# Kernel optimization log

Measured on AMD Instinct MI355X. Metric: run time of the kernel, lower is better.

Reference implementation:

```python
import jax, jax.numpy as jnp
import numpy as np

MODEL_DIM = 2048
HEAD_DIM = 64
STATE_DIM = 128
EXPAND = 2
CHUNK = 64
INNER = EXPAND * MODEL_DIM          # 4096
NHEADS = INNER // HEAD_DIM          # 64
IN_PROJ = INNER + 2 * STATE_DIM + NHEADS  # 4416
B_SZ = 2
SEQ = 4096


def segsum(x):
    """Stable segment sum: x (..., T) -> (..., T, T) with -inf above diagonal."""
    T = x.shape[-1]
    mask_strict = jnp.tril(jnp.ones((T, T), dtype=bool), -1)
    # element [d, e] = x[d] on strictly-lower triangle, 0 elsewhere
    xt = jnp.where(mask_strict, x[..., :, None], 0.0)
    seg = jnp.cumsum(xt, axis=-2)
    mask = jnp.tril(jnp.ones((T, T), dtype=bool), 0)
    return jnp.where(mask, seg, -jnp.inf)


def ssd(x, A, B, C, chunk):
    """Mamba-2 SSD. x:(b,L,h,p), A:(b,L,h), B/C:(b,L,n) shared over heads."""
    b, L, h, p = x.shape
    n = B.shape[-1]
    c = L // chunk
    x = x.reshape(b, c, chunk, h, p)
    A = A.reshape(b, c, chunk, h).transpose(0, 3, 1, 2)  # (b,h,c,l)
    B = B.reshape(b, c, chunk, n)
    C = C.reshape(b, c, chunk, n)

    A_cs = jnp.cumsum(A, axis=-1)                        # (b,h,c,l)
    Lm = jnp.exp(segsum(A))                              # (b,h,c,l,l)
    # 1. diagonal (intra-chunk) output
    Y_diag = jnp.einsum('bcln,bcsn,bhcls,bcshp->bclhp', C, B, Lm, x)
    # 2. per-chunk states
    decay_states = jnp.exp(A_cs[..., -1:] - A_cs)        # (b,h,c,l)
    states = jnp.einsum('bcln,bhcl,bclhp->bchpn', B, decay_states, x)
    states = jnp.concatenate([jnp.zeros_like(states[:, :1]), states], axis=1)
    # 3. inter-chunk recurrence
    A_chunk = jnp.pad(A_cs[..., -1], ((0, 0), (0, 0), (1, 0)))   # (b,h,c+1)
    decay_chunk = jnp.exp(segsum(A_chunk))               # (b,h,c+1,c+1)
    new_states = jnp.einsum('bhzc,bchpn->bzhpn', decay_chunk, states)
    states_prev, final_state = new_states[:, :-1], new_states[:, -1]
    # 4. state -> output
    Y_off = jnp.einsum('bcln,bchpn,bhcl->bclhp', C, states_prev, jnp.exp(A_cs))
    Y = (Y_diag + Y_off).reshape(b, L, h, p)
    return Y, final_state


def setup_inputs() -> dict:
    key = jax.random.key(0)
    ks = jax.random.split(key, 6)
    u = jax.random.normal(ks[0], (B_SZ, SEQ, MODEL_DIM), jnp.float32)
    W_in = jax.random.normal(ks[1], (IN_PROJ, MODEL_DIM), jnp.float32) * 0.02
    b_in = jnp.zeros((IN_PROJ,), jnp.float32)
    W_out = jax.random.normal(ks[2], (MODEL_DIM, INNER), jnp.float32) * 0.02
    b_out = jnp.zeros((MODEL_DIM,), jnp.float32)
    # A_log = log(uniform(1, 16)) per Mamba-2 init
    A_log = jnp.log(jax.random.uniform(ks[3], (NHEADS,), jnp.float32, 1.0, 16.0))
    # dt_bias = inv-softplus of dt ~ loguniform(1e-3, 1e-1)
    dt = jnp.exp(jax.random.uniform(ks[4], (NHEADS,), jnp.float32)
                 * (np.log(0.1) - np.log(0.001)) + np.log(0.001))
    dt = jnp.clip(dt, 1e-4, None)
    dt_bias = dt + jnp.log(-jnp.expm1(-dt))
    return {'u': u, 'W_in': W_in, 'b_in': b_in, 'W_out': W_out,
            'b_out': b_out, 'A_log': A_log, 'dt_bias': dt_bias}


def reference(u, W_in, b_in, W_out, b_out, A_log, dt_bias):
    xBCdt = u @ W_in.T + b_in                       # (b, L, IN_PROJ)
    x, Bm, Cm, dt = jnp.split(
        xBCdt, [INNER, INNER + STATE_DIM, INNER + 2 * STATE_DIM], axis=-1)
    A = -jnp.exp(A_log)                             # (h,)
    dt = jax.nn.softplus(dt + dt_bias)              # (b, L, h)
    x = x.reshape(B_SZ, SEQ, NHEADS, HEAD_DIM)
    y, final_state = ssd(x * dt[..., None], A * dt, Bm, Cm, CHUNK)
    y = y.reshape(B_SZ, SEQ, INNER)
    y = y @ W_out.T + b_out
    return y, final_state
```

## Files before the change

kernel.cpp:

```cpp
#include <hip/hip_runtime.h>
#include <hip/hip_bf16.h>

typedef __hip_bfloat16 bf16;
typedef __attribute__((ext_vector_type(8))) short short8;
typedef __attribute__((ext_vector_type(4))) float f32x4;

#define MODEL_DIM 2048
#define INNER     4096
#define NHEADS    64
#define HEAD_DIM  64
#define STATE_DIM 128
#define IN_PROJ   4416
#define NPAD      4608
#define BSZ       2
#define SEQ       4096
#define CHUNKL    64
#define NTOK      (BSZ*SEQ)
#define NCHUNK    (SEQ/CHUNKL)

#define WAITV0() asm volatile("s_waitcnt vmcnt(0)" ::: "memory")
#define BAR()    __builtin_amdgcn_s_barrier()
#define SCHEDB() __builtin_amdgcn_sched_barrier(0)
#define WAITLG(N) do { asm volatile("s_waitcnt lgkmcnt(" #N ")" ::: "memory"); SCHEDB(); } while (0)

#define SWZ(x) ((x) ^ ((((x) >> 7) & 7) << 4))

static __device__ __forceinline__ void gload_lds16(const bf16* g, bf16* l) {
  __builtin_amdgcn_global_load_lds((const __attribute__((address_space(1))) void*)g,
                                   (__attribute__((address_space(3))) void*)l, 16, 0, 0);
}

static __device__ __forceinline__ unsigned lds_u32(const void* p) {
  return (unsigned)(unsigned long long)(const __attribute__((address_space(3))) char*)p;
}

static __device__ __forceinline__ short8 ds_read128(unsigned addr) {
  short8 r;
  asm volatile("ds_read_b128 %0, %1" : "=v"(r) : "v"(addr));
  return r;
}

static __device__ __forceinline__ void stage_unit(const bf16* __restrict__ P, int K,
                                                  int blockRow, int kt,
                                                  char* region, int unit, int t) {
  int o = unit * 8192 + (t << 4);
  int lb = SWZ(o);
  int row = lb >> 7, colb = lb & 127;
  gload_lds16(P + (size_t)(blockRow + row) * K + kt + (colb >> 1), (bf16*)(region + o));
}

#define MFMA_BLK(MLO, MHI, NLO, NHI)                                                    \
  __builtin_amdgcn_s_setprio(1);                                                       \
  _Pragma("unroll") for (int mf = (MLO); mf < (MHI); ++mf)                             \
    _Pragma("unroll") for (int nf = (NLO); nf < (NHI); ++nf)                           \
      _Pragma("unroll") for (int ks = 0; ks < 2; ++ks)                                 \
        acc[mf][nf] = __builtin_amdgcn_mfma_f32_16x16x32_bf16(a[mf][ks], b[nf][ks],    \
                                                              acc[mf][nf], 0, 0, 0);  \
  __builtin_amdgcn_s_setprio(0);

template<int BN>
static __device__ __forceinline__ void gemm_core1(
    const bf16* __restrict__ Ag, const bf16* __restrict__ Bg,
    int K, int NT, int bm, int bn, char* lds, f32x4 (&acc)[8][BN / 64]) {
  constexpr int NR = BN / 64;
  constexpr int BB = 32768 + NR * 8192;
  const int t = threadIdx.x;
  const int lane = t & 63;
  const int wid = t >> 6, wm = wid >> 2, wn = wid & 3;
  const unsigned x16 = (unsigned)(lane & 7) << 4;
  const unsigned kb0 = (unsigned)(lane >> 4) << 4;
  const unsigned ldsB = lds_u32(lds);
  const unsigned aRow0 = (unsigned)(wm * 128 + (lane & 15)) * 128;
  const unsigned bRow0 = (unsigned)(wn * (BN / 4) + (lane & 15)) * 128;

#pragma unroll
  for (int u = 0; u < 4; ++u) stage_unit(Ag, K, bm, 0, lds, u, t);
#pragma unroll
  for (int u = 0; u < NR; ++u) stage_unit(Bg, K, bn, 0, lds + 32768, u, t);
  WAITV0();
  BAR();

  int cur = 0;
  for (int tt = 0; tt < NT; ++tt) {
    char* oth = lds + (cur ^ 1) * BB;
    const unsigned aB = ldsB + (unsigned)(cur * BB);
    const unsigned bB = aB + 32768;
    const bool st = (tt + 1 < NT);

    if (st) {
      const int kt1 = (tt + 1) * 64;
#pragma unroll
      for (int u = 0; u < 4; ++u) stage_unit(Ag, K, bm, kt1, oth, u, t);
#pragma unroll
      for (int u = 0; u < NR; ++u) stage_unit(Bg, K, bn, kt1, oth + 32768, u, t);
    }

    short8 a[8][2], b[NR][2];
#pragma unroll
    for (int mf = 0; mf < 4; ++mf)
#pragma unroll
      for (int ks = 0; ks < 2; ++ks)
        a[mf][ks] = ds_read128(aB + aRow0 + mf * 2048 + (((unsigned)(ks * 64) + kb0) ^ x16));
#pragma unroll
    for (int nf = 0; nf < 2; ++nf)
#pragma unroll
      for (int ks = 0; ks < 2; ++ks)
        b[nf][ks] = ds_read128(bB + bRow0 + nf * 2048 + (((unsigned)(ks * 64) + kb0) ^ x16));
#pragma unroll
    for (int mf = 4; mf < 8; ++mf)
#pragma unroll
      for (int ks = 0; ks < 2; ++ks)
        a[mf][ks] = ds_read128(aB + aRow0 + mf * 2048 + (((unsigned)(ks * 64) + kb0) ^ x16));
#pragma unroll
    for (int nf = 2; nf < NR; ++nf)
#pragma unroll
      for (int ks = 0; ks < 2; ++ks)
        b[nf][ks] = ds_read128(bB + bRow0 + nf * 2048 + (((unsigned)(ks * 64) + kb0) ^ x16));

    if constexpr (NR == 4) WAITLG(12); else WAITLG(10);
    MFMA_BLK(0, 4, 0, 2);
    if constexpr (NR == 4) WAITLG(4);  else WAITLG(2);
    MFMA_BLK(4, 8, 0, 2);
    WAITLG(0);
    MFMA_BLK(0, 8, 2, NR);

    if (st) WAITV0();
    BAR();
    cur ^= 1;
  }
}

__global__ __launch_bounds__(512, 2)
void gemm_in256(const bf16* __restrict__ A, const bf16* __restrict__ Bw,
                const float* __restrict__ bias, bf16* __restrict__ x_bf,
                bf16* __restrict__ B_bf, bf16* __restrict__ C_bf, float* __restrict__ dtraw) {
  __shared__ char lds[2 * (32768 + 3 * 8192)];
  int nwg = gridDim.x, bid = blockIdx.x;
  int cpx = nwg >> 3;
  int sb = (bid & 7) * cpx + (bid >> 3);
  int bx = sb % (NPAD / 192), by = sb / (NPAD / 192);
  int bm = by * 256, bn = bx * 192;
  f32x4 acc[8][3] = {};
  gemm_core1<192>(A, Bw, MODEL_DIM, MODEL_DIM / 64, bm, bn, lds, acc);
  const int lane = threadIdx.x & 63, wid = threadIdx.x >> 6;
  const int wm = wid >> 2, wn = wid & 3;
#pragma unroll
  for (int mf = 0; mf < 8; ++mf)
#pragma unroll
    for (int nf = 0; nf < 3; ++nf)
#pragma unroll
      for (int r = 0; r < 4; ++r) {
        int row = bm + wm * 128 + mf * 16 + (lane >> 4) * 4 + r;
        int col = bn + wn * 48 + nf * 16 + (lane & 15);
        float v = acc[mf][nf][r] + ((col < IN_PROJ) ? bias[col] : 0.f);
        if (col < 4096)       x_bf[(size_t)row * 4096 + col]         = __float2bfloat16(v);
        else if (col < 4224)  B_bf[(size_t)row * 128 + (col - 4096)] = __float2bfloat16(v);
        else if (col < 4352)  C_bf[(size_t)row * 128 + (col - 4224)] = __float2bfloat16(v);
        else if (col < 4416)  dtraw[(size_t)row * 64 + (col - 4352)] = v;
      }
}

__global__ __launch_bounds__(512, 2)
void gemm_out256(const bf16* __restrict__ A, const bf16* __restrict__ Bw,
                 const float* __restrict__ bias, float* __restrict__ C) {
  __shared__ char lds[2 * (32768 + 4 * 8192)];
  int nwg = gridDim.x, bid = blockIdx.x;
  int cpx = nwg >> 3;
  int sb = (bid & 7) * cpx + (bid >> 3);
  int bx = sb % (MODEL_DIM / 256), by = sb / (MODEL_DIM / 256);
  int bm = by * 256, bn = bx * 256;
  f32x4 acc[8][4] = {};
  gemm_core1<256>(A, Bw, INNER, INNER / 64, bm, bn, lds, acc);
  const int lane = threadIdx.x & 63, wid = threadIdx.x >> 6;
  const int wm = wid >> 2, wn = wid & 3;
#pragma unroll
  for (int mf = 0; mf < 8; ++mf)
#pragma unroll
    for (int nf = 0; nf < 4; ++nf)
#pragma unroll
      for (int r = 0; r < 4; ++r) {
        int row = bm + wm * 128 + mf * 16 + (lane >> 4) * 4 + r;
        int col = bn + wn * 64 + nf * 16 + (lane & 15);
        C[(size_t)row * MODEL_DIM + col] = acc[mf][nf][r] + bias[col];
      }
}

__global__ __launch_bounds__(256) void conv_f32_to_bf16(const float* __restrict__ src,
                                                        bf16* __restrict__ dst, int n4) {
  int i = blockIdx.x * 256 + threadIdx.x;
  if (i >= n4) return;
  float4 v = *(const float4*)(src + (size_t)i * 4);
  bf16* d = dst + (size_t)i * 4;
  d[0] = __float2bfloat16(v.x); d[1] = __float2bfloat16(v.y);
  d[2] = __float2bfloat16(v.z); d[3] = __float2bfloat16(v.w);
}

__global__ __launch_bounds__(256) void conv_win_pad(const float* __restrict__ W,
                                                    bf16* __restrict__ dst) {
  int i = blockIdx.x * 256 + threadIdx.x;
  int row = (i * 4) >> 11;
  int col = (i * 4) & 2047;
  bf16* d = dst + (size_t)i * 4;
  if (row < IN_PROJ) {
    float4 v = *(const float4*)(W + (size_t)row * 2048 + col);
    d[0] = __float2bfloat16(v.x); d[1] = __float2bfloat16(v.y);
    d[2] = __float2bfloat16(v.z); d[3] = __float2bfloat16(v.w);
  } else {
    bf16 z = __float2bfloat16(0.f);
    d[0] = z; d[1] = z; d[2] = z; d[3] = z;
  }
}

__global__ __launch_bounds__(256)
void prep_small(const float* __restrict__ dtraw, const float* __restrict__ A_log,
                const float* __restrict__ dt_bias, float* __restrict__ dts,
                float* __restrict__ a_dt) {
  int i = blockIdx.x * 256 + threadIdx.x;
  int h = i & 63;
  float z = dtraw[i] + dt_bias[h];
  float dt = (z > 20.f) ? z : log1pf(expf(z));
  dts[i] = dt;
  a_dt[i] = -expf(A_log[h]) * dt;
}

__global__ __launch_bounds__(256)
void ssd_states_kernel(const bf16* __restrict__ x_bf, const bf16* __restrict__ B_bf,
                       const float* __restrict__ dts, const float* __restrict__ a_dt,
                       float* __restrict__ acs_g, bf16* __restrict__ states_g) {
  __shared__ bf16 xT[64 * 64];
  __shared__ bf16 BdT[128 * 64];
  __shared__ float acs_s[64];
  int blk = blockIdx.x;
  int h = blk & 63, c = (blk >> 6) & 63, b = blk >> 12;
  int t = threadIdx.x, lane = t & 63, wid = t >> 6;
  int tokBase = b * SEQ + c * 64;

  if (t < 64) {
    float v = a_dt[(size_t)(tokBase + t) * 64 + h];
#pragma unroll
    for (int d = 1; d < 64; d <<= 1) { float o = __shfl_up(v, d); if (t >= d) v += o; }
    acs_s[t] = v;
    acs_g[(((size_t)(b * 64 + c)) * 64 + h) * 64 + t] = v;
  }
  __syncthreads();
  float acs63 = acs_s[63];

#pragma unroll
  for (int i = 0; i < 2; ++i) {
    int chunk = t + i * 256;
    int l = chunk >> 3, p0 = (chunk & 7) * 8;
    float dtv = dts[(size_t)(tokBase + l) * 64 + h];
    short8 vv = *(const short8*)(x_bf + (size_t)(tokBase + l) * 4096 + h * 64 + p0);
    const bf16* pv = (const bf16*)&vv;
#pragma unroll
    for (int j = 0; j < 8; ++j)
      xT[(p0 + j) * 64 + l] = __float2bfloat16(__bfloat162float(pv[j]) * dtv);
  }
#pragma unroll
  for (int i = 0; i < 4; ++i) {
    int chunk = t + i * 256;
    int l = chunk >> 4, n0 = (chunk & 15) * 8;
    float dec = expf(acs63 - acs_s[l]);
    short8 vv = *(const short8*)(B_bf + (size_t)(tokBase + l) * 128 + n0);
    const bf16* pv = (const bf16*)&vv;
#pragma unroll
    for (int j = 0; j < 8; ++j)
      BdT[(n0 + j) * 64 + l] = __float2bfloat16(__bfloat162float(pv[j]) * dec);
  }
  __syncthreads();

  int pBase = (wid >> 1) * 32, nBase = (wid & 1) * 64;
  f32x4 acc[2][4] = {};
#pragma unroll
  for (int ks = 0; ks < 2; ++ks) {
    short8 a[2], bb[4];
#pragma unroll
    for (int mi = 0; mi < 2; ++mi)
      a[mi] = *(const short8*)(xT + (pBase + mi * 16 + (lane & 15)) * 64 + ks * 32 + (lane >> 4) * 8);
#pragma unroll
    for (int ni = 0; ni < 4; ++ni)
      bb[ni] = *(const short8*)(BdT + (nBase + ni * 16 + (lane & 15)) * 64 + ks * 32 + (lane >> 4) * 8);
#pragma unroll
    for (int mi = 0; mi < 2; ++mi)
#pragma unroll
      for (int ni = 0; ni < 4; ++ni)
        acc[mi][ni] = __builtin_amdgcn_mfma_f32_16x16x32_bf16(a[mi], bb[ni], acc[mi][ni], 0, 0, 0);
  }
  size_t sbase = ((size_t)((b * 64 + c) * 64 + h)) * 64 * 128;
#pragma unroll
  for (int mi = 0; mi < 2; ++mi)
#pragma unroll
    for (int ni = 0; ni < 4; ++ni)
#pragma unroll
      for (int r = 0; r < 4; ++r) {
        int p = pBase + mi * 16 + (lane >> 4) * 4 + r;
        int n = nBase + ni * 16 + (lane & 15);
        states_g[sbase + (size_t)p * 128 + n] = __float2bfloat16(acc[mi][ni][r]);
      }
}

__global__ __launch_bounds__(256)
void ssd_scan_kernel(bf16* __restrict__ states_g, const float* __restrict__ acs_g,
                     float* __restrict__ out_fs) {
  int blk = blockIdx.x;
  int q = blk & 3, bh = blk >> 2;
  int b = bh >> 6, h = bh & 63;
  int t = threadIdx.x;
  int eb = q * 2048 + t;
  float S[8];
#pragma unroll
  for (int i = 0; i < 8; ++i) S[i] = 0.f;
  for (int c = 0; c < 64; ++c) {
    size_t base = ((size_t)((b * 64 + c) * 64 + h)) * 8192;
    float dfac = expf(acs_g[(((size_t)(b * 64 + c)) * 64 + h) * 64 + 63]);
#pragma unroll
    for (int i = 0; i < 8; ++i) {
      int e = eb + i * 256;
      float cs = __bfloat162float(states_g[base + e]);
      states_g[base + e] = __float2bfloat16(S[i]);
      S[i] = dfac * S[i] + cs;
    }
  }
  size_t ob = (size_t)bh * 8192;
#pragma unroll
  for (int i = 0; i < 8; ++i) out_fs[ob + eb + i * 256] = S[i];
}

__global__ __launch_bounds__(256)
void ssd_out_kernel(bf16* __restrict__ x_bf, const bf16* __restrict__ B_bf,
                    const bf16* __restrict__ C_bf, const float* __restrict__ dts,
                    const float* __restrict__ acs_g, const bf16* __restrict__ states_g) {
  __shared__ bf16 Cs[64 * 128];
  __shared__ bf16 BsMs[64 * 128];
  __shared__ bf16 xT[64 * 64];
  __shared__ bf16 Sp[64 * 128];
  __shared__ float acs_s[64];
  int blk = blockIdx.x;
  int h = blk & 63, c = (blk >> 6) & 63, b = blk >> 12;
  int t = threadIdx.x, lane = t & 63, wid = t >> 6;
  int tokBase = b * SEQ + c * 64;
  size_t sbase = ((size_t)((b * 64 + c) * 64 + h)) * 8192;

  if (t < 64) acs_s[t] = acs_g[(((size_t)(b * 64 + c)) * 64 + h) * 64 + t];
#pragma unroll
  for (int i = 0; i < 4; ++i) {
    int chunk = t + i * 256;
    int l = chunk >> 4, n0 = (chunk & 15) * 8;
    *(short8*)(Cs + l * 128 + n0) = *(const short8*)(C_bf + (size_t)(tokBase + l) * 128 + n0);
    *(short8*)(BsMs + l * 128 + n0) = *(const short8*)(B_bf + (size_t)(tokBase + l) * 128 + n0);
  }
#pragma unroll
  for (int i = 0; i < 2; ++i) {
    int chunk = t + i * 256;
    int l = chunk >> 3, p0 = (chunk & 7) * 8;
    float dtv = dts[(size_t)(tokBase + l) * 64 + h];
    short8 vv = *(const short8*)(x_bf + (size_t)(tokBase + l) * 4096 + h * 64 + p0);
    const bf16* pv = (const bf16*)&vv;
#pragma unroll
    for (int j = 0; j < 8; ++j)
      xT[(p0 + j) * 64 + l] = __float2bfloat16(__bfloat162float(pv[j]) * dtv);
  }
#pragma unroll
  for (int i = 0; i < 4; ++i) {
    int chunk = t + i * 256;
    *(short8*)(Sp + chunk * 8) = *(const short8*)(states_g + sbase + chunk * 8);
  }
  __syncthreads();

  int lBase = (wid >> 1) * 32, sBase = (wid & 1) * 32;
  f32x4 g[2][2] = {};
#pragma unroll
  for (int ks = 0; ks < 4; ++ks) {
    short8 a[2], bb[2];
#pragma unroll
    for (int mi = 0; mi < 2; ++mi)
      a[mi] = *(const short8*)(Cs + (lBase + mi * 16 + (lane & 15)) * 128 + ks * 32 + (lane >> 4) * 8);
#pragma unroll
    for (int ni = 0; ni < 2; ++ni)
      bb[ni] = *(const short8*)(BsMs + (sBase + ni * 16 + (lane & 15)) * 128 + ks * 32 + (lane >> 4) * 8);
#pragma unroll
    for (int mi = 0; mi < 2; ++mi)
#pragma unroll
      for (int ni = 0; ni < 2; ++ni)
        g[mi][ni] = __builtin_amdgcn_mfma_f32_16x16x32_bf16(a[mi], bb[ni], g[mi][ni], 0, 0, 0);
  }
  __syncthreads();

  bf16* Ms = BsMs;
#pragma unroll
  for (int mi = 0; mi < 2; ++mi)
#pragma unroll
    for (int ni = 0; ni < 2; ++ni)
#pragma unroll
      for (int r = 0; r < 4; ++r) {
        int row = lBase + mi * 16 + (lane >> 4) * 4 + r;
        int col = sBase + ni * 16 + (lane & 15);
        float lm = (row >= col) ? expf(acs_s[row] - acs_s[col]) : 0.f;
        Ms[row * 64 + col] = __float2bfloat16(g[mi][ni][r] * lm);
      }
  __syncthreads();

  int pBase = (wid & 1) * 32;
  f32x4 yd[2][2] = {}, yo[2][2] = {};
#pragma unroll
  for (int ks = 0; ks < 2; ++ks) {
    short8 a[2], bb[2];
#pragma unroll
    for (int mi = 0; mi < 2; ++mi)
      a[mi] = *(const short8*)(Ms + (lBase + mi * 16 + (lane & 15)) * 64 + ks * 32 + (lane >> 4) * 8);
#pragma unroll
    for (int ni = 0; ni < 2; ++ni)
      bb[ni] = *(const short8*)(xT + (pBase + ni * 16 + (lane & 15)) * 64 + ks * 32 + (lane >> 4) * 8);
#pragma unroll
    for (int mi = 0; mi < 2; ++mi)
#pragma unroll
      for (int ni = 0; ni < 2; ++ni)
        yd[mi][ni] = __builtin_amdgcn_mfma_f32_16x16x32_bf16(a[mi], bb[ni], yd[mi][ni], 0, 0, 0);
  }
#pragma unroll
  for (int ks = 0; ks < 4; ++ks) {
    short8 a[2], bb[2];
#pragma unroll
    for (int mi = 0; mi < 2; ++mi)
      a[mi] = *(const short8*)(Cs + (lBase + mi * 16 + (lane & 15)) * 128 + ks * 32 + (lane >> 4) * 8);
#pragma unroll
    for (int ni = 0; ni < 2; ++ni)
      bb[ni] = *(const short8*)(Sp + (pBase + ni * 16 + (lane & 15)) * 128 + ks * 32 + (lane >> 4) * 8);
#pragma unroll
    for (int mi = 0; mi < 2; ++mi)
#pragma unroll
      for (int ni = 0; ni < 2; ++ni)
        yo[mi][ni] = __builtin_amdgcn_mfma_f32_16x16x32_bf16(a[mi], bb[ni], yo[mi][ni], 0, 0, 0);
  }
  __syncthreads();
#pragma unroll
  for (int mi = 0; mi < 2; ++mi)
#pragma unroll
    for (int ni = 0; ni < 2; ++ni)
#pragma unroll
      for (int r = 0; r < 4; ++r) {
        int lr = lBase + mi * 16 + (lane >> 4) * 4 + r;
        int p = pBase + ni * 16 + (lane & 15);
        float val = yd[mi][ni][r] + expf(acs_s[lr]) * yo[mi][ni][r];
        x_bf[(size_t)(tokBase + lr) * 4096 + h * 64 + p] = __float2bfloat16(val);
      }
}

extern "C" void kernel_launch(void* const* d_in, const int* in_sizes, int n_in,
                              void* d_out, int out_size, void* d_ws, size_t ws_size,
                              hipStream_t stream) {
  const float* u       = (const float*)d_in[0];
  const float* W_in    = (const float*)d_in[1];
  const float* b_in    = (const float*)d_in[2];
  const float* W_out   = (const float*)d_in[3];
  const float* b_out   = (const float*)d_in[4];
  const float* A_log   = (const float*)d_in[5];
  const float* dt_bias = (const float*)d_in[6];

  float* y_out  = (float*)d_out;
  float* fs_out = y_out + (size_t)NTOK * MODEL_DIM;

  char* ws = (char*)d_ws;
  size_t off = 0;
  auto alloc = [&](size_t bytes) { char* p = ws + off; off += (bytes + 255) & ~255ull; return p; };
  bf16*  wout_bf = (bf16*) alloc((size_t)MODEL_DIM * INNER * 2);
  bf16*  x_bf    = (bf16*) alloc((size_t)NTOK * INNER * 2);
  bf16*  B_bf    = (bf16*) alloc((size_t)NTOK * STATE_DIM * 2);
  bf16*  C_bf    = (bf16*) alloc((size_t)NTOK * STATE_DIM * 2);
  float* dtraw   = (float*)alloc((size_t)NTOK * NHEADS * 4);
  float* dts     = (float*)alloc((size_t)NTOK * NHEADS * 4);
  float* a_dt    = (float*)alloc((size_t)NTOK * NHEADS * 4);
  float* acs     = (float*)alloc((size_t)BSZ * NCHUNK * NHEADS * 64 * 4);
  char*  Q       = alloc((size_t)BSZ * NCHUNK * NHEADS * 64 * 128 * 2);
  bf16*  states  = (bf16*)Q;
  bf16*  u_bf    = (bf16*)Q;
  bf16*  win_bf  = u_bf + (size_t)NTOK * MODEL_DIM;
  (void)ws_size; (void)off; (void)in_sizes; (void)n_in; (void)out_size;

  conv_f32_to_bf16<<<dim3(16384), dim3(256), 0, stream>>>(u, u_bf, NTOK * MODEL_DIM / 4);
  conv_win_pad<<<dim3(NPAD * MODEL_DIM / 1024), dim3(256), 0, stream>>>(W_in, win_bf);
  conv_f32_to_bf16<<<dim3(8192), dim3(256), 0, stream>>>(W_out, wout_bf, MODEL_DIM * INNER / 4);

  gemm_in256<<<dim3((NTOK / 256) * (NPAD / 192)), dim3(512), 0, stream>>>(
      u_bf, win_bf, b_in, x_bf, B_bf, C_bf, dtraw);

  prep_small<<<dim3(NTOK * NHEADS / 256), dim3(256), 0, stream>>>(dtraw, A_log, dt_bias, dts, a_dt);

  ssd_states_kernel<<<dim3(BSZ * NCHUNK * NHEADS), dim3(256), 0, stream>>>(
      x_bf, B_bf, dts, a_dt, acs, states);

  ssd_scan_kernel<<<dim3(BSZ * NHEADS * 4), dim3(256), 0, stream>>>(states, acs, fs_out);

  ssd_out_kernel<<<dim3(BSZ * NCHUNK * NHEADS), dim3(256), 0, stream>>>(
      x_bf, B_bf, C_bf, dts, acs, states);

  gemm_out256<<<dim3((MODEL_DIM / 256) * (NTOK / 256)), dim3(512), 0, stream>>>(
      x_bf, wout_bf, b_out, y_out);
}
```

Before: 584.2 us.

## Software-pipeline LDS fragment reads across k-iterations in the GEMM core

```diff
diff --git a/kernel.cpp b/kernel.cpp
--- a/kernel.cpp
+++ b/kernel.cpp
@@ -49,17 +49,17 @@
   gload_lds16(P + (size_t)(blockRow + row) * K + kt + (colb >> 1), (bf16*)(region + o));
 }
 
-#define MFMA_BLK(MLO, MHI, NLO, NHI)                                                    \
-  __builtin_amdgcn_s_setprio(1);                                                       \
-  _Pragma("unroll") for (int mf = (MLO); mf < (MHI); ++mf)                             \
-    _Pragma("unroll") for (int nf = (NLO); nf < (NHI); ++nf)                           \
-      _Pragma("unroll") for (int ks = 0; ks < 2; ++ks)                                 \
-        acc[mf][nf] = __builtin_amdgcn_mfma_f32_16x16x32_bf16(a[mf][ks], b[nf][ks],    \
-                                                              acc[mf][nf], 0, 0, 0);  \
+#define MFMA_CH(av, MBASE, NLO, NHI)                                                    \
+  __builtin_amdgcn_s_setprio(1);                                                        \
+  _Pragma("unroll") for (int mf = 0; mf < 4; ++mf)                                      \
+    _Pragma("unroll") for (int nf = (NLO); nf < (NHI); ++nf)                            \
+      _Pragma("unroll") for (int ks = 0; ks < 2; ++ks)                                  \
+        acc[(MBASE) + mf][nf] = __builtin_amdgcn_mfma_f32_16x16x32_bf16(                \
+            av[mf][ks], b[nf][ks], acc[(MBASE) + mf][nf], 0, 0, 0);                     \
   __builtin_amdgcn_s_setprio(0);
 
 template<int BN>
-static __device__ __forceinline__ void gemm_core1(
+static __device__ __forceinline__ void gemm_core2(
     const bf16* __restrict__ Ag, const bf16* __restrict__ Bg,
     int K, int NT, int bm, int bn, char* lds, f32x4 (&acc)[8][BN / 64]) {
   constexpr int NR = BN / 64;
@@ -80,12 +80,35 @@
   WAITV0();
   BAR();
 
-  int cur = 0;
+  short8 aN[4][2], ah[4][2], b[NR][2];
+#pragma unroll
+  for (int mf = 0; mf < 4; ++mf)
+#pragma unroll
+    for (int ks = 0; ks < 2; ++ks)
+      aN[mf][ks] = ds_read128(ldsB + aRow0 + mf * 2048 + (((unsigned)(ks * 64) + kb0) ^ x16));
+
   for (int tt = 0; tt < NT; ++tt) {
-    char* oth = lds + (cur ^ 1) * BB;
-    const unsigned aB = ldsB + (unsigned)(cur * BB);
-    const unsigned bB = aB + 32768;
+    const unsigned aB  = ldsB + (unsigned)((tt & 1) * BB);
+    const unsigned bB  = aB + 32768;
+    const unsigned aB1 = ldsB + (unsigned)(((tt + 1) & 1) * BB);
+    char* oth = lds + ((tt + 1) & 1) * BB;
     const bool st = (tt + 1 < NT);
+
+#pragma unroll
+    for (int nf = 0; nf < 2; ++nf)
+#pragma unroll
+      for (int ks = 0; ks < 2; ++ks)
+        b[nf][ks] = ds_read128(bB + bRow0 + nf * 2048 + (((unsigned)(ks * 64) + kb0) ^ x16));
+#pragma unroll
+    for (int nf = 2; nf < NR; ++nf)
+#pragma unroll
+      for (int ks = 0; ks < 2; ++ks)
+        b[nf][ks] = ds_read128(bB + bRow0 + nf * 2048 + (((unsigned)(ks * 64) + kb0) ^ x16));
+#pragma unroll
+    for (int mf = 0; mf < 4; ++mf)
+#pragma unroll
+      for (int ks = 0; ks < 2; ++ks)
+        ah[mf][ks] = ds_read128(aB + aRow0 + (4 + mf) * 2048 + (((unsigned)(ks * 64) + kb0) ^ x16));
 
     if (st) {
       const int kt1 = (tt + 1) * 64;
@@ -95,38 +118,25 @@
       for (int u = 0; u < NR; ++u) stage_unit(Bg, K, bn, kt1, oth + 32768, u, t);
     }
 
-    short8 a[8][2], b[NR][2];
-#pragma unroll
-    for (int mf = 0; mf < 4; ++mf)
-#pragma unroll
-      for (int ks = 0; ks < 2; ++ks)
-        a[mf][ks] = ds_read128(aB + aRow0 + mf * 2048 + (((unsigned)(ks * 64) + kb0) ^ x16));
-#pragma unroll
-    for (int nf = 0; nf < 2; ++nf)
-#pragma unroll
-      for (int ks = 0; ks < 2; ++ks)
-        b[nf][ks] = ds_read128(bB + bRow0 + nf * 2048 + (((unsigned)(ks * 64) + kb0) ^ x16));
-#pragma unroll
-    for (int mf = 4; mf < 8; ++mf)
-#pragma unroll
-      for (int ks = 0; ks < 2; ++ks)
-        a[mf][ks] = ds_read128(aB + aRow0 + mf * 2048 + (((unsigned)(ks * 64) + kb0) ^ x16));
-#pragma unroll
-    for (int nf = 2; nf < NR; ++nf)
-#pragma unroll
-      for (int ks = 0; ks < 2; ++ks)
-        b[nf][ks] = ds_read128(bB + bRow0 + nf * 2048 + (((unsigned)(ks * 64) + kb0) ^ x16));
-
     if constexpr (NR == 4) WAITLG(12); else WAITLG(10);
-    MFMA_BLK(0, 4, 0, 2);
-    if constexpr (NR == 4) WAITLG(4);  else WAITLG(2);
-    MFMA_BLK(4, 8, 0, 2);
-    WAITLG(0);
-    MFMA_BLK(0, 8, 2, NR);
-
-    if (st) WAITV0();
+    MFMA_CH(aN, 0, 0, 2);
+    WAITLG(8);
+    MFMA_CH(aN, 0, 2, NR);
+
+    WAITV0();
     BAR();
-    cur ^= 1;
+    if (st) {
+#pragma unroll
+      for (int mf = 0; mf < 4; ++mf)
+#pragma unroll
+        for (int ks = 0; ks < 2; ++ks)
+          aN[mf][ks] = ds_read128(aB1 + aRow0 + mf * 2048 + (((unsigned)(ks * 64) + kb0) ^ x16));
+      WAITLG(8);
+    } else {
+      WAITLG(0);
+    }
+    MFMA_CH(ah, 4, 0, NR);
+    BAR();
   }
 }
 
@@ -141,7 +151,7 @@
   int bx = sb % (NPAD / 192), by = sb / (NPAD / 192);
   int bm = by * 256, bn = bx * 192;
   f32x4 acc[8][3] = {};
-  gemm_core1<192>(A, Bw, MODEL_DIM, MODEL_DIM / 64, bm, bn, lds, acc);
+  gemm_core2<192>(A, Bw, MODEL_DIM, MODEL_DIM / 64, bm, bn, lds, acc);
   const int lane = threadIdx.x & 63, wid = threadIdx.x >> 6;
   const int wm = wid >> 2, wn = wid & 3;
 #pragma unroll
@@ -170,7 +180,7 @@
   int bx = sb % (MODEL_DIM / 256), by = sb / (MODEL_DIM / 256);
   int bm = by * 256, bn = bx * 256;
   f32x4 acc[8][4] = {};
-  gemm_core1<256>(A, Bw, INNER, INNER / 64, bm, bn, lds, acc);
+  gemm_core2<256>(A, Bw, INNER, INNER / 64, bm, bn, lds, acc);
   const int lane = threadIdx.x & 63, wid = threadIdx.x >> 6;
   const int wm = wid >> 2, wn = wid & 3;
 #pragma unroll
```

Result: slower. 600.6 us (+2.8%).

## Fuse chunk-state computation with inter-chunk scan into one sequential kernel

Applied to the files above, without the earlier changes.

```diff
diff --git a/kernel.cpp b/kernel.cpp
--- a/kernel.cpp
+++ b/kernel.cpp
@@ -223,107 +223,112 @@
   a_dt[i] = -expf(A_log[h]) * dt;
 }
 
+#define LP 72
 __global__ __launch_bounds__(256)
-void ssd_states_kernel(const bf16* __restrict__ x_bf, const bf16* __restrict__ B_bf,
-                       const float* __restrict__ dts, const float* __restrict__ a_dt,
-                       float* __restrict__ acs_g, bf16* __restrict__ states_g) {
-  __shared__ bf16 xT[64 * 64];
-  __shared__ bf16 BdT[128 * 64];
-  __shared__ float acs_s[64];
+void ssd_fused_kernel(const bf16* __restrict__ x_bf, const bf16* __restrict__ B_bf,
+                      const float* __restrict__ dts_g, const float* __restrict__ a_dt,
+                      float* __restrict__ acs_g, bf16* __restrict__ states_g,
+                      float* __restrict__ out_fs) {
+  __shared__ bf16 xT[2][32 * LP];
+  __shared__ bf16 BT[2][128 * LP];
+  __shared__ float sc_s[64];
+  __shared__ float dfac_s[1];
   int blk = blockIdx.x;
-  int h = blk & 63, c = (blk >> 6) & 63, b = blk >> 12;
-  int t = threadIdx.x, lane = t & 63, wid = t >> 6;
-  int tokBase = b * SEQ + c * 64;
-
-  if (t < 64) {
-    float v = a_dt[(size_t)(tokBase + t) * 64 + h];
-#pragma unroll
-    for (int d = 1; d < 64; d <<= 1) { float o = __shfl_up(v, d); if (t >= d) v += o; }
-    acs_s[t] = v;
-    acs_g[(((size_t)(b * 64 + c)) * 64 + h) * 64 + t] = v;
-  }
-  __syncthreads();
-  float acs63 = acs_s[63];
-
-#pragma unroll
-  for (int i = 0; i < 2; ++i) {
-    int chunk = t + i * 256;
-    int l = chunk >> 3, p0 = (chunk & 7) * 8;
-    float dtv = dts[(size_t)(tokBase + l) * 64 + h];
-    short8 vv = *(const short8*)(x_bf + (size_t)(tokBase + l) * 4096 + h * 64 + p0);
-    const bf16* pv = (const bf16*)&vv;
-#pragma unroll
-    for (int j = 0; j < 8; ++j)
-      xT[(p0 + j) * 64 + l] = __float2bfloat16(__bfloat162float(pv[j]) * dtv);
-  }
-#pragma unroll
-  for (int i = 0; i < 4; ++i) {
-    int chunk = t + i * 256;
-    int l = chunk >> 4, n0 = (chunk & 15) * 8;
-    float dec = expf(acs63 - acs_s[l]);
-    short8 vv = *(const short8*)(B_bf + (size_t)(tokBase + l) * 128 + n0);
-    const bf16* pv = (const bf16*)&vv;
-#pragma unroll
-    for (int j = 0; j < 8; ++j)
-      BdT[(n0 + j) * 64 + l] = __float2bfloat16(__bfloat162float(pv[j]) * dec);
-  }
-  __syncthreads();
-
-  int pBase = (wid >> 1) * 32, nBase = (wid & 1) * 64;
-  f32x4 acc[2][4] = {};
-#pragma unroll
-  for (int ks = 0; ks < 2; ++ks) {
-    short8 a[2], bb[4];
-#pragma unroll
-    for (int mi = 0; mi < 2; ++mi)
-      a[mi] = *(const short8*)(xT + (pBase + mi * 16 + (lane & 15)) * 64 + ks * 32 + (lane >> 4) * 8);
-#pragma unroll
-    for (int ni = 0; ni < 4; ++ni)
-      bb[ni] = *(const short8*)(BdT + (nBase + ni * 16 + (lane & 15)) * 64 + ks * 32 + (lane >> 4) * 8);
-#pragma unroll
-    for (int mi = 0; mi < 2; ++mi)
-#pragma unroll
-      for (int ni = 0; ni < 4; ++ni)
-        acc[mi][ni] = __builtin_amdgcn_mfma_f32_16x16x32_bf16(a[mi], bb[ni], acc[mi][ni], 0, 0, 0);
-  }
-  size_t sbase = ((size_t)((b * 64 + c) * 64 + h)) * 64 * 128;
-#pragma unroll
-  for (int mi = 0; mi < 2; ++mi)
-#pragma unroll
-    for (int ni = 0; ni < 4; ++ni)
+  int pg = blk & 1, h = (blk >> 1) & 63, b = blk >> 7;
+  int t = threadIdx.x, lane = t & 63, w = t >> 6;
+  int lx = t >> 2, sx = t & 3;
+  int lB = t >> 2, sB = t & 3;
+
+  f32x4 S4[4] = {};
+  short8 rx, rB[4]; float ra = 0.f, rdt = 0.f;
+  {
+    int tb = b * SEQ;
+    rx = *(const short8*)(x_bf + (size_t)(tb + lx) * 4096 + h * 64 + pg * 32 + sx * 8);
+#pragma unroll
+    for (int k = 0; k < 4; ++k)
+      rB[k] = *(const short8*)(B_bf + (size_t)(tb + lB) * 128 + sB * 32 + k * 8);
+    if (t < 64) { ra = a_dt[(size_t)(tb + t) * 64 + h]; rdt = dts_g[(size_t)(tb + t) * 64 + h]; }
+  }
+
+  for (int c = 0; c < 64; ++c) {
+    int cn = (c < 63) ? c + 1 : 63;
+    int tbn = b * SEQ + cn * 64;
+    short8 rx2 = *(const short8*)(x_bf + (size_t)(tbn + lx) * 4096 + h * 64 + pg * 32 + sx * 8);
+    short8 rB2[4];
+#pragma unroll
+    for (int k = 0; k < 4; ++k)
+      rB2[k] = *(const short8*)(B_bf + (size_t)(tbn + lB) * 128 + sB * 32 + k * 8);
+    float ra2 = 0.f, rdt2 = 0.f;
+    if (t < 64) { ra2 = a_dt[(size_t)(tbn + t) * 64 + h]; rdt2 = dts_g[(size_t)(tbn + t) * 64 + h]; }
+
+    if (t < 64) {
+      float v = ra;
+#pragma unroll
+      for (int d = 1; d < 64; d <<= 1) { float o = __shfl_up(v, d); if (t >= d) v += o; }
+      float a63 = __shfl(v, 63);
+      if (pg == 0) acs_g[(((size_t)(b * 64 + c)) * 64 + h) * 64 + t] = v;
+      sc_s[t] = rdt * expf(a63 - v);
+      if (t == 0) dfac_s[0] = expf(a63);
+    }
+    __syncthreads();
+
+    int bufc = c & 1;
+    float dfac = dfac_s[0];
+    {
+      float s_l = sc_s[lx];
+      const bf16* pv = (const bf16*)&rx;
+#pragma unroll
+      for (int j = 0; j < 8; ++j)
+        xT[bufc][(sx * 8 + j) * LP + lx] = __float2bfloat16(__bfloat162float(pv[j]) * s_l);
+#pragma unroll
+      for (int k = 0; k < 4; ++k) {
+        const bf16* pb = (const bf16*)&rB[k];
+        int n0 = sB * 32 + k * 8;
+#pragma unroll
+        for (int j = 0; j < 8; ++j) BT[bufc][(n0 + j) * LP + lB] = pb[j];
+      }
+    }
+    __syncthreads();
+
+    int ps = (w >> 1) * 16, nb = (w & 1) * 64;
+    f32x4 acc[4] = {};
+    short8 af[2];
+#pragma unroll
+    for (int ks = 0; ks < 2; ++ks)
+      af[ks] = *(const short8*)(&xT[bufc][(ps + (lane & 15)) * LP + ks * 32 + (lane >> 4) * 8]);
+#pragma unroll
+    for (int nf = 0; nf < 4; ++nf)
+#pragma unroll
+      for (int ks = 0; ks < 2; ++ks) {
+        short8 bf_ = *(const short8*)(&BT[bufc][(nb + nf * 16 + (lane & 15)) * LP + ks * 32 + (lane >> 4) * 8]);
+        acc[nf] = __builtin_amdgcn_mfma_f32_16x16x32_bf16(af[ks], bf_, acc[nf], 0, 0, 0);
+      }
+    size_t sbase = ((size_t)((b * 64 + c) * 64 + h)) * 8192;
+#pragma unroll
+    for (int nf = 0; nf < 4; ++nf)
 #pragma unroll
       for (int r = 0; r < 4; ++r) {
-        int p = pBase + mi * 16 + (lane >> 4) * 4 + r;
-        int n = nBase + ni * 16 + (lane & 15);
-        states_g[sbase + (size_t)p * 128 + n] = __float2bfloat16(acc[mi][ni][r]);
-      }
-}
-
-__global__ __launch_bounds__(256)
-void ssd_scan_kernel(bf16* __restrict__ states_g, const float* __restrict__ acs_g,
-                     float* __restrict__ out_fs) {
-  int blk = blockIdx.x;
-  int q = blk & 3, bh = blk >> 2;
-  int b = bh >> 6, h = bh & 63;
-  int t = threadIdx.x;
-  int eb = q * 2048 + t;
-  float S[8];
-#pragma unroll
-  for (int i = 0; i < 8; ++i) S[i] = 0.f;
-  for (int c = 0; c < 64; ++c) {
-    size_t base = ((size_t)((b * 64 + c) * 64 + h)) * 8192;
-    float dfac = expf(acs_g[(((size_t)(b * 64 + c)) * 64 + h) * 64 + 63]);
-#pragma unroll
-    for (int i = 0; i < 8; ++i) {
-      int e = eb + i * 256;
-      float cs = __bfloat162float(states_g[base + e]);
-      states_g[base + e] = __float2bfloat16(S[i]);
-      S[i] = dfac * S[i] + cs;
+        int p = pg * 32 + ps + (lane >> 4) * 4 + r;
+        int n = nb + nf * 16 + (lane & 15);
+        states_g[sbase + (size_t)p * 128 + n] = __float2bfloat16(S4[nf][r]);
+        S4[nf][r] = dfac * S4[nf][r] + acc[nf][r];
+      }
+
+    rx = rx2; ra = ra2; rdt = rdt2;
+#pragma unroll
+    for (int k = 0; k < 4; ++k) rB[k] = rB2[k];
+  }
+
+  size_t ob = ((size_t)(b * 64 + h)) * 8192;
+  int ps = (w >> 1) * 16, nb = (w & 1) * 64;
+#pragma unroll
+  for (int nf = 0; nf < 4; ++nf)
+#pragma unroll
+    for (int r = 0; r < 4; ++r) {
+      int p = pg * 32 + ps + (lane >> 4) * 4 + r;
+      int n = nb + nf * 16 + (lane & 15);
+      out_fs[ob + (size_t)p * 128 + n] = S4[nf][r];
     }
-  }
-  size_t ob = (size_t)bh * 8192;
-#pragma unroll
-  for (int i = 0; i < 8; ++i) out_fs[ob + eb + i * 256] = S[i];
 }
 
 __global__ __launch_bounds__(256)
@@ -486,10 +491,8 @@
 
   prep_small<<<dim3(NTOK * NHEADS / 256), dim3(256), 0, stream>>>(dtraw, A_log, dt_bias, dts, a_dt);
 
-  ssd_states_kernel<<<dim3(BSZ * NCHUNK * NHEADS), dim3(256), 0, stream>>>(
-      x_bf, B_bf, dts, a_dt, acs, states);
-
-  ssd_scan_kernel<<<dim3(BSZ * NHEADS * 4), dim3(256), 0, stream>>>(states, acs, fs_out);
+  ssd_fused_kernel<<<dim3(BSZ * NHEADS * 2), dim3(256), 0, stream>>>(
+      x_bf, B_bf, dts, a_dt, acs, states, fs_out);
 
   ssd_out_kernel<<<dim3(BSZ * NCHUNK * NHEADS), dim3(256), 0, stream>>>(
       x_bf, B_bf, C_bf, dts, acs, states);
```

Result: no change. 573.4 us (-1.9%).
